# Optimization experiments

Measured on AMD Instinct MI355X. Metric: run time of the kernel, lower is better.

Reference implementation:

```python
import jax, jax.numpy as jnp
import numpy as np

EPS = 1e-7        # keras backend.epsilon()
TEMPERATURE = 0.1
MOMENTUM = 0.9
CENTROID_LR = 0.1
REPULSION_STRENGTH = 0.1
MIN_DISTANCE = 1.0

B, S, D = 8, 4096, 512
K = 512


def setup_inputs() -> dict:
    key = jax.random.key(0)
    kx, kc = jax.random.split(key)
    x = jax.random.normal(kx, (B, S, D), dtype=jnp.float32)
    # GlorotNormal for (K, D) centroid table
    glorot_std = float(np.sqrt(2.0 / (K + D)))
    centroids = jax.random.normal(kc, (K, D), dtype=jnp.float32) * glorot_std
    centroid_momentum = jnp.zeros((K, D), dtype=jnp.float32)
    return {"x": x, "centroids": centroids, "centroid_momentum": centroid_momentum}


def reference(x, centroids, centroid_momentum):
    # ---- flatten non-feature dims: (B, S, D) -> (N, D) ----
    flat = x.reshape(-1, x.shape[-1])                      # (N, D)

    # ---- squared Euclidean distances to centroids (GEMM form) ----
    x_sq = jnp.sum(flat * flat, axis=-1, keepdims=True)    # (N, 1)
    c_sq = jnp.sum(centroids * centroids, axis=-1)         # (K,)
    cross = flat @ centroids.T                             # (N, K)
    distances = x_sq + c_sq[None, :] - 2.0 * cross         # (N, K)

    # ---- temperature-scaled soft assignments (stable softmax w/ eps) ----
    scaled = -distances / TEMPERATURE
    scaled = scaled - jnp.max(scaled, axis=-1, keepdims=True)
    exp_d = jnp.exp(scaled)
    assignments = exp_d / (jnp.sum(exp_d, axis=-1, keepdims=True) + EPS)  # (N, K)

    # ---- soft K-means centroid targets ----
    sum_w = jnp.sum(assignments, axis=0)                   # (K,)
    weighted_sum = assignments.T @ flat                    # (K, D)
    new_centroids = weighted_sum / (sum_w[:, None] + EPS)  # (K, D)

    # ---- pairwise centroid repulsion ----
    diffs = centroids[:, None, :] - centroids[None, :, :]  # (K, K, D)
    sq_dist = jnp.sum(diffs * diffs, axis=-1)              # (K, K)
    dist = jnp.sqrt(sq_dist + EPS)
    rep_w = jnp.maximum(0.0, 1.0 - dist / MIN_DISTANCE)
    rep_scale = (REPULSION_STRENGTH * rep_w / (dist + EPS))[..., None]
    repulsion = jnp.sum(rep_scale * diffs, axis=1)         # (K, D)

    # ---- momentum update of centroids ----
    updates = new_centroids - centroids + repulsion
    mom_new = MOMENTUM * centroid_momentum + (1.0 - MOMENTUM) * updates
    centroids_new = centroids + CENTROID_LR * mom_new

    # ---- output: assignments reshaped to (B, S, K) ----
    out = assignments.reshape(x.shape[:-1] + (assignments.shape[-1],))
    return out, centroids_new, mom_new
```

## Files before the change

kernel.cpp:

```cpp
#include <hip/hip_runtime.h>
#include <hip/hip_bf16.h>

#define EPSF 1e-7f

typedef __attribute__((ext_vector_type(8))) short bf16x8;
typedef __attribute__((ext_vector_type(4))) float f32x4v;

__device__ inline ushort f2bf_bits(float x) {
    union { __hip_bfloat16 b; ushort u; } cv;
    cv.b = __float2bfloat16(x);
    return cv.u;
}
__device__ inline float bfbits2f(ushort u) {
    union { ushort u; __hip_bfloat16 b; } cv;
    cv.u = u;
    return __bfloat162float(cv.b);
}
__device__ inline void split2(float x, ushort& h, ushort& l) {
    h = f2bf_bits(x);
    l = f2bf_bits(x - bfbits2f(h));
}
__device__ inline uint4 pack8(const ushort* h) {
    uint4 p;
    p.x = (uint)h[0] | ((uint)h[1] << 16);
    p.y = (uint)h[2] | ((uint)h[3] << 16);
    p.z = (uint)h[4] | ((uint)h[5] << 16);
    p.w = (uint)h[6] | ((uint)h[7] << 16);
    return p;
}

__device__ inline void gload_lds16(const ushort* g, ushort* l) {
    __builtin_amdgcn_global_load_lds(
        (const __attribute__((address_space(1))) unsigned int*)g,
        (__attribute__((address_space(3))) unsigned int*)l, 16, 0, 0);
}

__global__ __launch_bounds__(256) void csqc_v3(const float* __restrict__ C,
                                               float* __restrict__ csq,
                                               ushort* __restrict__ Chl) {
    const int wave = threadIdx.x >> 6, lane = threadIdx.x & 63;
    const int row = blockIdx.x * 4 + wave;
    const int kc = lane >> 2, s = lane & 3;
    const float* p = C + row * 512 + lane * 8;
    float4 a = *(const float4*)p;
    float4 b = *(const float4*)(p + 4);
    float v[8] = {a.x, a.y, a.z, a.w, b.x, b.y, b.z, b.w};
    ushort h[8], l[8];
    float sqs = 0.f;
#pragma unroll
    for (int i = 0; i < 8; ++i) {
        sqs += v[i] * v[i];
        split2(v[i], h[i], l[i]);
    }
    ushort* base = Chl + (long)row * 1024 + kc * 64 + s * 8;
    *(uint4*)base = pack8(h);
    *(uint4*)(base + 32) = pack8(l);
#pragma unroll
    for (int off = 1; off < 64; off <<= 1) sqs += __shfl_xor(sqs, off, 64);
    if (lane == 0) csq[row] = sqs;
}

__global__ __launch_bounds__(512) void logsm(const float* __restrict__ X,
                                             const ushort* __restrict__ Chl,
                                             const float* __restrict__ csq,
                                             float* __restrict__ assign,
                                             ushort* __restrict__ Abf,
                                             ushort* __restrict__ Xh,
                                             float* __restrict__ sum_w) {
    __shared__ __align__(16) ushort sA[64 * 64];
    __shared__ __align__(16) ushort sB[512 * 64];
    __shared__ float rmaxs[64][4];
    __shared__ float rsums[64][4];
    __shared__ float swacc[512];
    const int tid = threadIdx.x;
    const int m0 = ((blockIdx.x & 7) * 64 + (blockIdx.x >> 3)) * 64;
    const int wid = tid >> 6, lane = tid & 63;
    const int wm = wid >> 2, wn = wid & 3;
    const int lrow = lane & 15, lkb = lane >> 4;
    swacc[tid] = 0.f;
    f32x4v acc[2][8] = {};

    const int ar = tid >> 3, aq = tid & 7;
    const float* xrow = X + (long)(m0 + ar) * 512 + aq * 4;
    float4 v = *(const float4*)xrow;

#pragma unroll 1
    for (int kc = 0; kc < 16; ++kc) {
        __syncthreads();
        {
            ushort h[4], l[4];
            split2(v.x, h[0], l[0]);
            split2(v.y, h[1], l[1]);
            split2(v.z, h[2], l[2]);
            split2(v.w, h[3], l[3]);
            ushort4 hv = {h[0], h[1], h[2], h[3]};
            ushort4 lv = {l[0], l[1], l[2], l[3]};
            const int sh = (aq >> 1) ^ (ar & 7);
            const int slo = ((aq >> 1) + 4) ^ (ar & 7);
            *(ushort4*)&sA[ar * 64 + (sh << 3) + (aq & 1) * 4] = hv;
            *(ushort4*)&sA[ar * 64 + (slo << 3) + (aq & 1) * 4] = lv;
            *(ushort4*)(Xh + (long)(m0 + ar) * 512 + kc * 32 + aq * 4) = hv;
        }
#pragma unroll
        for (int i = 0; i < 8; ++i) {
            const int sl = i * 512 + tid;
            const int r = sl >> 3, j = sl & 7;
            const int s = j ^ (r & 7);
            gload_lds16(Chl + (long)r * 1024 + kc * 64 + s * 8,
                        &sB[(i * 512 + wid * 64) * 8]);
        }
        if (kc < 15) v = *(const float4*)(xrow + (kc + 1) * 32);
        __syncthreads();
        bf16x8 ah[2], al[2];
#pragma unroll
        for (int mi = 0; mi < 2; ++mi) {
            const int R = wm * 32 + mi * 16 + lrow;
            ah[mi] = *(const bf16x8*)&sA[R * 64 + ((lkb ^ (R & 7)) << 3)];
            al[mi] = *(const bf16x8*)&sA[R * 64 + (((lkb + 4) ^ (R & 7)) << 3)];
        }
#pragma unroll
        for (int ni = 0; ni < 8; ++ni) {
            const int Rn = wn * 128 + ni * 16 + lrow;
            bf16x8 bh = *(const bf16x8*)&sB[Rn * 64 + ((lkb ^ (Rn & 7)) << 3)];
            bf16x8 bl = *(const bf16x8*)&sB[Rn * 64 + (((lkb + 4) ^ (Rn & 7)) << 3)];
#pragma unroll
            for (int mi = 0; mi < 2; ++mi) {
                acc[mi][ni] = __builtin_amdgcn_mfma_f32_16x16x32_bf16(ah[mi], bh, acc[mi][ni], 0, 0, 0);
                acc[mi][ni] = __builtin_amdgcn_mfma_f32_16x16x32_bf16(ah[mi], bl, acc[mi][ni], 0, 0, 0);
                acc[mi][ni] = __builtin_amdgcn_mfma_f32_16x16x32_bf16(al[mi], bh, acc[mi][ni], 0, 0, 0);
            }
        }
    }
    const int colb = wn * 128 + lrow;
    float cs[8];
#pragma unroll
    for (int ni = 0; ni < 8; ++ni) cs[ni] = csq[colb + ni * 16];
    float mx[2][4];
#pragma unroll
    for (int mi = 0; mi < 2; ++mi)
#pragma unroll
        for (int r = 0; r < 4; ++r) {
            float m = -3.0e38f;
#pragma unroll
            for (int ni = 0; ni < 8; ++ni) {
                float l = 2.0f * acc[mi][ni][r] - cs[ni];
                acc[mi][ni][r] = l;
                m = fmaxf(m, l);
            }
            mx[mi][r] = m;
        }
#pragma unroll
    for (int off = 1; off < 16; off <<= 1)
#pragma unroll
        for (int mi = 0; mi < 2; ++mi)
#pragma unroll
            for (int r = 0; r < 4; ++r) mx[mi][r] = fmaxf(mx[mi][r], __shfl_xor(mx[mi][r], off, 64));
    if (lrow == 0) {
#pragma unroll
        for (int mi = 0; mi < 2; ++mi)
#pragma unroll
            for (int r = 0; r < 4; ++r) rmaxs[wm * 32 + mi * 16 + lkb * 4 + r][wn] = mx[mi][r];
    }
    __syncthreads();
    float gmax[2][4];
#pragma unroll
    for (int mi = 0; mi < 2; ++mi)
#pragma unroll
        for (int r = 0; r < 4; ++r) {
            const int row = wm * 32 + mi * 16 + lkb * 4 + r;
            gmax[mi][r] = fmaxf(fmaxf(rmaxs[row][0], rmaxs[row][1]),
                                fmaxf(rmaxs[row][2], rmaxs[row][3]));
        }
    float sm[2][4] = {};
#pragma unroll
    for (int mi = 0; mi < 2; ++mi)
#pragma unroll
        for (int ni = 0; ni < 8; ++ni)
#pragma unroll
            for (int r = 0; r < 4; ++r) {
                float e = expf((acc[mi][ni][r] - gmax[mi][r]) * 10.0f);
                acc[mi][ni][r] = e;
                sm[mi][r] += e;
            }
#pragma unroll
    for (int off = 1; off < 16; off <<= 1)
#pragma unroll
        for (int mi = 0; mi < 2; ++mi)
#pragma unroll
            for (int r = 0; r < 4; ++r) sm[mi][r] += __shfl_xor(sm[mi][r], off, 64);
    if (lrow == 0) {
#pragma unroll
        for (int mi = 0; mi < 2; ++mi)
#pragma unroll
            for (int r = 0; r < 4; ++r) rsums[wm * 32 + mi * 16 + lkb * 4 + r][wn] = sm[mi][r];
    }
    __syncthreads();
    float inv[2][4];
#pragma unroll
    for (int mi = 0; mi < 2; ++mi)
#pragma unroll
        for (int r = 0; r < 4; ++r) {
            const int row = wm * 32 + mi * 16 + lkb * 4 + r;
            float t = rsums[row][0] + rsums[row][1] + rsums[row][2] + rsums[row][3];
            inv[mi][r] = 1.0f / (t + EPSF);
        }
    float csum[8] = {};
#pragma unroll
    for (int mi = 0; mi < 2; ++mi)
#pragma unroll
        for (int ni = 0; ni < 8; ++ni) {
            const int col = colb + ni * 16;
#pragma unroll
            for (int r = 0; r < 4; ++r) {
                const int row = wm * 32 + mi * 16 + lkb * 4 + r;
                float a = acc[mi][ni][r] * inv[mi][r];
                assign[(long)(m0 + row) * 512 + col] = a;
                Abf[(long)(m0 + row) * 512 + col] = f2bf_bits(a);
                csum[ni] += a;
            }
        }
#pragma unroll
    for (int off = 16; off < 64; off <<= 1)
#pragma unroll
        for (int ni = 0; ni < 8; ++ni) csum[ni] += __shfl_xor(csum[ni], off, 64);
    if (lkb == 0) {
#pragma unroll
        for (int ni = 0; ni < 8; ++ni) atomicAdd(&swacc[colb + ni * 16], csum[ni]);
    }
    __syncthreads();
    atomicAdd(&sum_w[tid], swacc[tid]);
}

__global__ __launch_bounds__(256) void gram_s_v3(const ushort* __restrict__ Chl,
                                                 const float* __restrict__ csq,
                                                 float* __restrict__ S,
                                                 float* __restrict__ rsum) {
    __shared__ __align__(16) ushort sA[128 * 64];
    __shared__ __align__(16) ushort sB[128 * 64];
    __shared__ float rs_s[128];
    const int tid = threadIdx.x;
    const int n0 = blockIdx.x * 128;
    const int m0 = blockIdx.y * 128;
    const int wid = tid >> 6, lane = tid & 63;
    const int wm = wid >> 1, wn = wid & 1;
    const int lrow = lane & 15, lkb = lane >> 4;
    f32x4v acc[4][4] = {};

#pragma unroll 1
    for (int kc = 0; kc < 16; ++kc) {
        __syncthreads();
#pragma unroll
        for (int i = 0; i < 4; ++i) {
            const int sl = wid * 256 + i * 64 + lane;
            const int r = sl >> 3, j = sl & 7;
            const int s = j ^ (r & 7);
            gload_lds16(Chl + (long)(m0 + r) * 1024 + kc * 64 + s * 8,
                        &sA[(wid * 256 + i * 64) * 8]);
            gload_lds16(Chl + (long)(n0 + r) * 1024 + kc * 64 + s * 8,
                        &sB[(wid * 256 + i * 64) * 8]);
        }
        __syncthreads();
        bf16x8 ah[4], al[4], bh[4], bl[4];
#pragma unroll
        for (int mi = 0; mi < 4; ++mi) {
            const int R = wm * 64 + mi * 16 + lrow;
            ah[mi] = *(const bf16x8*)&sA[R * 64 + ((lkb ^ (R & 7)) << 3)];
            al[mi] = *(const bf16x8*)&sA[R * 64 + (((lkb + 4) ^ (R & 7)) << 3)];
        }
#pragma unroll
        for (int ni = 0; ni < 4; ++ni) {
            const int R = wn * 64 + ni * 16 + lrow;
            bh[ni] = *(const bf16x8*)&sB[R * 64 + ((lkb ^ (R & 7)) << 3)];
            bl[ni] = *(const bf16x8*)&sB[R * 64 + (((lkb + 4) ^ (R & 7)) << 3)];
        }
#pragma unroll
        for (int mi = 0; mi < 4; ++mi)
#pragma unroll
            for (int ni = 0; ni < 4; ++ni) {
                acc[mi][ni] = __builtin_amdgcn_mfma_f32_16x16x32_bf16(ah[mi], bh[ni], acc[mi][ni], 0, 0, 0);
                acc[mi][ni] = __builtin_amdgcn_mfma_f32_16x16x32_bf16(ah[mi], bl[ni], acc[mi][ni], 0, 0, 0);
                acc[mi][ni] = __builtin_amdgcn_mfma_f32_16x16x32_bf16(al[mi], bh[ni], acc[mi][ni], 0, 0, 0);
            }
    }
    if (tid < 128) rs_s[tid] = 0.f;
    __syncthreads();
    const int colb = n0 + wn * 64 + lrow;
    float csj[4];
#pragma unroll
    for (int ni = 0; ni < 4; ++ni) csj[ni] = csq[colb + ni * 16];
#pragma unroll
    for (int mi = 0; mi < 4; ++mi) {
        const int rowb = m0 + wm * 64 + mi * 16 + lkb * 4;
#pragma unroll
        for (int r = 0; r < 4; ++r) {
            const int row = rowb + r;
            const float csi = csq[row];
            float rowpart = 0.f;
#pragma unroll
            for (int ni = 0; ni < 4; ++ni) {
                const int col = colb + ni * 16;
                float sq = csi + csj[ni] - 2.0f * acc[mi][ni][r];
                float dist = sqrtf(fmaxf(sq, 0.f) + EPSF);
                float w = fmaxf(0.f, 1.f - dist);
                float sval = (row == col) ? 0.f : (0.1f * w / (dist + EPSF));
                S[(long)row * 512 + col] = sval;
                rowpart += sval;
            }
            atomicAdd(&rs_s[row - m0], rowpart);
        }
    }
    __syncthreads();
    if (tid < 128) atomicAdd(&rsum[m0 + tid], rs_s[tid]);
}

__global__ __launch_bounds__(256) void wsum_v3(const ushort* __restrict__ Abf,
                                               const ushort* __restrict__ Xh,
                                               float* __restrict__ WSp) {
    __shared__ __align__(16) ushort sA[2][128 * 64];
    __shared__ __align__(16) ushort sB[2][128 * 64];
    const int tid = threadIdx.x;
    const int lin = blockIdx.x + blockIdx.y * 4 + blockIdx.z * 16;
    const int T = (lin & 7) * 64 + (lin >> 3);
    const int k0 = (T & 3) * 128;
    const int d0 = ((T >> 2) & 3) * 128;
    const int zc = T >> 4;
    const long n0 = (long)zc * 1024;
    const int wid = tid >> 6, lane = tid & 63;
    const int wm = wid >> 1, wn = wid & 1;
    const int lrow = lane & 15, lkb = lane >> 4;
    f32x4v acc[4][4] = {};

    const int c0_ = tid & 127, no0 = tid >> 7;
    ushort ha[4][8], hx[4][8];

#define WSUM_LOAD(NCOFF)                                                      \
    {                                                                          \
        _Pragma("unroll")                                                      \
        for (int it = 0; it < 4; ++it) {                                       \
            const int idx = it * 256 + tid;                                    \
            const int c = idx & 127;                                           \
            const int no = idx >> 7;                                           \
            const long nb = n0 + (NCOFF) + (long)no * 8;                       \
            _Pragma("unroll")                                                  \
            for (int jj = 0; jj < 8; ++jj) {                                   \
                ha[it][jj] = Abf[(nb + jj) * 512 + k0 + c];                    \
                hx[it][jj] = Xh[(nb + jj) * 512 + d0 + c];                     \
            }                                                                  \
        }                                                                      \
    }
#define WSUM_WRITE(B)                                                         \
    {                                                                          \
        _Pragma("unroll")                                                      \
        for (int it = 0; it < 4; ++it) {                                       \
            const int idx = it * 256 + tid;                                    \
            const int c = idx & 127;                                           \
            const int no = idx >> 7;                                           \
            const int sl = no ^ (c & 7);                                       \
            *(uint4*)&sA[(B)][c * 64 + sl * 8] = pack8(ha[it]);                \
            *(uint4*)&sB[(B)][c * 64 + sl * 8] = pack8(hx[it]);                \
        }                                                                      \
    }

    WSUM_LOAD(0);
    WSUM_WRITE(0);
    int cur = 0;
#pragma unroll 1
    for (int nc = 0; nc < 16; ++nc) {
        if (nc < 15) WSUM_LOAD((nc + 1) * 64);
        __syncthreads();
#pragma unroll
        for (int kk = 0; kk < 2; ++kk) {
            const int j = kk * 4 + lkb;
            bf16x8 af[4], bfv[4];
#pragma unroll
            for (int mi = 0; mi < 4; ++mi) {
                const int R = wm * 64 + mi * 16 + lrow;
                af[mi] = *(const bf16x8*)&sA[cur][R * 64 + ((j ^ (R & 7)) << 3)];
            }
#pragma unroll
            for (int ni = 0; ni < 4; ++ni) {
                const int R = wn * 64 + ni * 16 + lrow;
                bfv[ni] = *(const bf16x8*)&sB[cur][R * 64 + ((j ^ (R & 7)) << 3)];
            }
#pragma unroll
            for (int mi = 0; mi < 4; ++mi)
#pragma unroll
                for (int ni = 0; ni < 4; ++ni)
                    acc[mi][ni] = __builtin_amdgcn_mfma_f32_16x16x32_bf16(af[mi], bfv[ni], acc[mi][ni], 0, 0, 0);
        }
        if (nc < 15) WSUM_WRITE(cur ^ 1);
        cur ^= 1;
    }
    float* dst = WSp + (size_t)zc * 262144;
#pragma unroll
    for (int mi = 0; mi < 4; ++mi) {
        const int k = k0 + wm * 64 + mi * 16 + lkb * 4;
#pragma unroll
        for (int ni = 0; ni < 4; ++ni) {
            const int d = d0 + wn * 64 + ni * 16 + lrow;
#pragma unroll
            for (int r = 0; r < 4; ++r)
                dst[(k + r) * 512 + d] = acc[mi][ni][r];
        }
    }
#undef WSUM_LOAD
#undef WSUM_WRITE
}

__global__ __launch_bounds__(256) void apply_update(const float* __restrict__ Cent,
                                                    const float* __restrict__ Mom,
                                                    const float* __restrict__ S,
                                                    const float* __restrict__ rsum,
                                                    const float* __restrict__ WSp,
                                                    const float* __restrict__ sum_w,
                                                    float* __restrict__ outC,
                                                    float* __restrict__ outM) {
    const int i = blockIdx.x;
    __shared__ float srow[512];
    __shared__ int nz;
    const int tid = threadIdx.x;
    if (tid == 0) nz = 0;
    __syncthreads();
    float2 sv = *(const float2*)(S + (long)i * 512 + tid * 2);
    srow[tid * 2] = sv.x;
    srow[tid * 2 + 1] = sv.y;
    if (sv.x != 0.f || sv.y != 0.f) nz = 1;
    __syncthreads();
    const float rs = rsum[i];
    const float invw = 1.0f / (sum_w[i] + EPSF);
    const int d0 = tid * 2;
    float ws0 = 0.f, ws1 = 0.f;
#pragma unroll 4
    for (int z = 0; z < 32; ++z) {
        float2 w = *(const float2*)(WSp + (size_t)z * 262144 + (long)i * 512 + d0);
        ws0 += w.x;
        ws1 += w.y;
    }
    float sc0 = 0.f, sc1 = 0.f;
    if (nz) {
        for (int j = 0; j < 512; ++j) {
            const float s = srow[j];
            if (s != 0.f) {
                sc0 += s * Cent[(long)j * 512 + d0];
                sc1 += s * Cent[(long)j * 512 + d0 + 1];
            }
        }
    }
    float2 ci = *(const float2*)(Cent + (long)i * 512 + d0);
    float2 mo = *(const float2*)(Mom + (long)i * 512 + d0);
    float rep0 = rs * ci.x - sc0;
    float rep1 = rs * ci.y - sc1;
    float mn0 = 0.9f * mo.x + 0.1f * (ws0 * invw - ci.x + rep0);
    float mn1 = 0.9f * mo.y + 0.1f * (ws1 * invw - ci.y + rep1);
    float2 om = {mn0, mn1};
    float2 oc = {ci.x + 0.1f * mn0, ci.y + 0.1f * mn1};
    *(float2*)(outM + (long)i * 512 + d0) = om;
    *(float2*)(outC + (long)i * 512 + d0) = oc;
}

__global__ __launch_bounds__(256) void csq_only(const float* __restrict__ C,
                                                float* __restrict__ csq) {
    const int wave = threadIdx.x >> 6, lane = threadIdx.x & 63;
    const int row = blockIdx.x * 4 + wave;
    const float* p = C + row * 512 + lane * 8;
    float4 a = *(const float4*)p;
    float4 b = *(const float4*)(p + 4);
    float s = a.x * a.x + a.y * a.y + a.z * a.z + a.w * a.w +
              b.x * b.x + b.y * b.y + b.z * b.z + b.w * b.w;
#pragma unroll
    for (int off = 1; off < 64; off <<= 1) s += __shfl_xor(s, off, 64);
    if (lane == 0) csq[row] = s;
}

__global__ __launch_bounds__(256) void logits_mfma(const float* __restrict__ X,
                                                   const float* __restrict__ Cm,
                                                   const float* __restrict__ csq,
                                                   float* __restrict__ L) {
    __shared__ ushort sAh[128][64];
    __shared__ ushort sAl[128][64];
    __shared__ ushort sBh[128][64];
    __shared__ ushort sBl[128][64];
    const int tid = threadIdx.x;
    const int m0 = blockIdx.x * 128;
    const int n0 = blockIdx.y * 128;
    const int wid = tid >> 6, lane = tid & 63;
    const int wm = wid >> 1, wn = wid & 1;
    const int lrow = lane & 15;
    const int lkb = lane >> 4;
    f32x4v acc[4][4] = {};
    for (int k0 = 0; k0 < 512; k0 += 64) {
        __syncthreads();
#pragma unroll
        for (int s = 0; s < 8; ++s) {
            const int idx = s * 256 + tid;
            const int r = idx >> 4;
            const int c4 = (idx & 15) << 2;
            const int e = c4 ^ ((r & 7) << 3);
            float4 va = *(const float4*)(X + (long)(m0 + r) * 512 + k0 + c4);
            ushort4 hh, ll;
            split2(va.x, hh.x, ll.x);
            split2(va.y, hh.y, ll.y);
            split2(va.z, hh.z, ll.z);
            split2(va.w, hh.w, ll.w);
            *(ushort4*)&sAh[r][e] = hh;
            *(ushort4*)&sAl[r][e] = ll;
            float4 vb = *(const float4*)(Cm + (long)(n0 + r) * 512 + k0 + c4);
            split2(vb.x, hh.x, ll.x);
            split2(vb.y, hh.y, ll.y);
            split2(vb.z, hh.z, ll.z);
            split2(vb.w, hh.w, ll.w);
            *(ushort4*)&sBh[r][e] = hh;
            *(ushort4*)&sBl[r][e] = ll;
        }
        __syncthreads();
#pragma unroll
        for (int kk = 0; kk < 2; ++kk) {
            const int ebase = kk * 32 + lkb * 8;
            bf16x8 ah[4], al[4], bh[4], bl[4];
#pragma unroll
            for (int mi = 0; mi < 4; ++mi) {
                const int R = wm * 64 + mi * 16 + lrow;
                const int e = ebase ^ ((R & 7) << 3);
                ah[mi] = *(const bf16x8*)&sAh[R][e];
                al[mi] = *(const bf16x8*)&sAl[R][e];
            }
#pragma unroll
            for (int ni = 0; ni < 4; ++ni) {
                const int Rn = wn * 64 + ni * 16 + lrow;
                const int e = ebase ^ ((Rn & 7) << 3);
                bh[ni] = *(const bf16x8*)&sBh[Rn][e];
                bl[ni] = *(const bf16x8*)&sBl[Rn][e];
            }
#pragma unroll
            for (int mi = 0; mi < 4; ++mi)
#pragma unroll
                for (int ni = 0; ni < 4; ++ni) {
                    acc[mi][ni] = __builtin_amdgcn_mfma_f32_16x16x32_bf16(ah[mi], bh[ni], acc[mi][ni], 0, 0, 0);
                    acc[mi][ni] = __builtin_amdgcn_mfma_f32_16x16x32_bf16(ah[mi], bl[ni], acc[mi][ni], 0, 0, 0);
                    acc[mi][ni] = __builtin_amdgcn_mfma_f32_16x16x32_bf16(al[mi], bh[ni], acc[mi][ni], 0, 0, 0);
                }
        }
    }
    const int colb = n0 + wn * 64 + lrow;
    float cs[4];
#pragma unroll
    for (int ni = 0; ni < 4; ++ni) cs[ni] = csq[colb + ni * 16];
#pragma unroll
    for (int mi = 0; mi < 4; ++mi) {
        const int rowb = m0 + wm * 64 + mi * 16 + lkb * 4;
#pragma unroll
        for (int r = 0; r < 4; ++r) {
            float* Lp = L + (long)(rowb + r) * 512 + colb;
#pragma unroll
            for (int ni = 0; ni < 4; ++ni)
                Lp[ni * 16] = 2.0f * acc[mi][ni][r] - cs[ni];
        }
    }
}

__global__ __launch_bounds__(256) void softmax_rows(float* __restrict__ L,
                                                    float* __restrict__ sum_w,
                                                    ushort* __restrict__ Abf) {
    __shared__ float swacc[512];
    const int tid = threadIdx.x;
    for (int i = tid; i < 512; i += 256) swacc[i] = 0.f;
    __syncthreads();
    const int wave = tid >> 6, lane = tid & 63;
    float racc[8] = {};
    for (int r = blockIdx.x * 4 + wave; r < 32768; r += 2048) {
        float* p = L + (long)r * 512 + lane * 8;
        float4 v0 = *(float4*)p;
        float4 v1 = *(float4*)(p + 4);
        float v[8] = {v0.x, v0.y, v0.z, v0.w, v1.x, v1.y, v1.z, v1.w};
        float m = v[0];
#pragma unroll
        for (int i = 1; i < 8; ++i) m = fmaxf(m, v[i]);
#pragma unroll
        for (int off = 1; off < 64; off <<= 1) m = fmaxf(m, __shfl_xor(m, off, 64));
        float e[8], s = 0.f;
#pragma unroll
        for (int i = 0; i < 8; ++i) {
            e[i] = expf((v[i] - m) * 10.0f);
            s += e[i];
        }
#pragma unroll
        for (int off = 1; off < 64; off <<= 1) s += __shfl_xor(s, off, 64);
        const float inv = 1.0f / (s + EPSF);
        ushort eb[8];
#pragma unroll
        for (int i = 0; i < 8; ++i) {
            e[i] *= inv;
            racc[i] += e[i];
            eb[i] = f2bf_bits(e[i]);
        }
        float4 o0 = {e[0], e[1], e[2], e[3]};
        float4 o1 = {e[4], e[5], e[6], e[7]};
        *(float4*)p = o0;
        *(float4*)(p + 4) = o1;
        if (Abf) *(uint4*)(Abf + (long)r * 512 + lane * 8) = pack8(eb);
    }
#pragma unroll
    for (int i = 0; i < 8; ++i) atomicAdd(&swacc[lane * 8 + i], racc[i]);
    __syncthreads();
    for (int i = tid; i < 512; i += 256) atomicAdd(&sum_w[i], swacc[i]);
}

__global__ __launch_bounds__(256) void gemm_wsum(const float* __restrict__ A,
                                                 const float* __restrict__ X,
                                                 float* __restrict__ WS) {
    __shared__ float As[16][64];
    __shared__ float Xs[16][64];
    const int tid = threadIdx.x;
    const int tx = tid & 15, ty = tid >> 4;
    const int lrow = tid >> 4;
    const int lcol = (tid & 15) << 2;
    const int k0 = blockIdx.x * 64;
    const int d0 = blockIdx.y * 64;
    const int n0 = blockIdx.z * 1024;
    float acc[4][4] = {};
    for (int nc = 0; nc < 1024; nc += 16) {
        const long nrow = n0 + nc + lrow;
        float4 av = *(const float4*)(A + nrow * 512 + k0 + lcol);
        float4 xv = *(const float4*)(X + nrow * 512 + d0 + lcol);
        __syncthreads();
        *(float4*)&As[lrow][lcol] = av;
        *(float4*)&Xs[lrow][lcol] = xv;
        __syncthreads();
#pragma unroll
        for (int nn = 0; nn < 16; ++nn) {
            float4 a = *(const float4*)&As[nn][ty << 2];
            float4 x = *(const float4*)&Xs[nn][tx << 2];
            float aa[4] = {a.x, a.y, a.z, a.w};
            float xx[4] = {x.x, x.y, x.z, x.w};
#pragma unroll
            for (int i = 0; i < 4; ++i)
#pragma unroll
                for (int j = 0; j < 4; ++j) acc[i][j] += aa[i] * xx[j];
        }
    }
#pragma unroll
    for (int i = 0; i < 4; ++i)
#pragma unroll
        for (int j = 0; j < 4; ++j)
            atomicAdd(&WS[(k0 + (ty << 2) + i) * 512 + d0 + (tx << 2) + j], acc[i][j]);
}

__global__ __launch_bounds__(256) void repulse_update(const float* __restrict__ Cent,
                                                      const float* __restrict__ Mom,
                                                      const float* __restrict__ csq,
                                                      const float* __restrict__ WS,
                                                      const float* __restrict__ sum_w,
                                                      float* __restrict__ outC,
                                                      float* __restrict__ outM) {
    const int i = blockIdx.x;
    __shared__ float ci[512];
    __shared__ float rep[512];
    const int tid = threadIdx.x, wave = tid >> 6, lane = tid & 63;
    for (int d = tid; d < 512; d += 256) {
        ci[d] = Cent[i * 512 + d];
        rep[d] = 0.f;
    }
    __syncthreads();
    float cil[8];
#pragma unroll
    for (int m = 0; m < 8; ++m) cil[m] = ci[lane * 8 + m];
    const float csqi = csq[i];
    float racc[8] = {};
    for (int j = wave; j < 512; j += 4) {
        if (j == i) continue;
        const float* cj = Cent + j * 512 + lane * 8;
        float4 c0 = *(const float4*)cj;
        float4 c1 = *(const float4*)(cj + 4);
        float cjl[8] = {c0.x, c0.y, c0.z, c0.w, c1.x, c1.y, c1.z, c1.w};
        float dot = 0.f;
#pragma unroll
        for (int m = 0; m < 8; ++m) dot += cil[m] * cjl[m];
#pragma unroll
        for (int off = 1; off < 64; off <<= 1) dot += __shfl_xor(dot, off, 64);
        float sq = csqi + csq[j] - 2.f * dot;
        float dist = sqrtf(fmaxf(sq, 0.f) + EPSF);
        float w = fmaxf(0.f, 1.f - dist);
        float scale = 0.1f * w / (dist + EPSF);
#pragma unroll
        for (int m = 0; m < 8; ++m) racc[m] += scale * (cil[m] - cjl[m]);
    }
#pragma unroll
    for (int m = 0; m < 8; ++m) atomicAdd(&rep[lane * 8 + m], racc[m]);
    __syncthreads();
    const float invw = 1.0f / (sum_w[i] + EPSF);
    for (int d = tid; d < 512; d += 256) {
        float nc = WS[i * 512 + d] * invw;
        float upd = nc - ci[d] + rep[d];
        float mn = 0.9f * Mom[i * 512 + d] + 0.1f * upd;
        outM[i * 512 + d] = mn;
        outC[i * 512 + d] = ci[d] + 0.1f * mn;
    }
}

extern "C" void kernel_launch(void* const* d_in, const int* in_sizes, int n_in,
                              void* d_out, int out_size, void* d_ws, size_t ws_size,
                              hipStream_t stream) {
    const float* X = (const float*)d_in[0];
    const float* C = (const float*)d_in[1];
    const float* M = (const float*)d_in[2];
    float* out = (float*)d_out;
    float* assign = out;
    float* outC = out + 16777216;
    float* outM = outC + 262144;

    char* wsb = (char*)d_ws;
    const size_t MB = 1024ull * 1024ull;
    float* WS = (float*)wsb;
    float* sum_w = (float*)(wsb + 1 * MB);
    float* rsum = (float*)(wsb + 1 * MB + 2048);
    float* csq = (float*)(wsb + 1 * MB + 4096);
    ushort* Chl = (ushort*)(wsb + 2 * MB);
    float* S = (float*)(wsb + 3 * MB);
    float* WSp = (float*)(wsb + 4 * MB);
    ushort* Xh = (ushort*)(wsb + 36 * MB);
    ushort* Abf = (ushort*)(wsb + 100 * MB);
    const size_t NEED = 132 * MB;

    if (ws_size >= NEED) {
        hipMemsetAsync(wsb + 1 * MB, 0, 4096, stream);
        csqc_v3<<<128, 256, 0, stream>>>(C, csq, Chl);
        gram_s_v3<<<dim3(4, 4), 256, 0, stream>>>(Chl, csq, S, rsum);
        logsm<<<512, 512, 0, stream>>>(X, Chl, csq, assign, Abf, Xh, sum_w);
        wsum_v3<<<dim3(4, 4, 32), 256, 0, stream>>>(Abf, Xh, WSp);
        apply_update<<<512, 256, 0, stream>>>(C, M, S, rsum, WSp, sum_w, outC, outM);
    } else {
        hipMemsetAsync(d_ws, 0, 1 * MB + 8192, stream);
        csq_only<<<128, 256, 0, stream>>>(C, csq);
        logits_mfma<<<dim3(256, 4), 256, 0, stream>>>(X, C, csq, assign);
        softmax_rows<<<512, 256, 0, stream>>>(assign, sum_w, nullptr);
        gemm_wsum<<<dim3(8, 8, 32), 256, 0, stream>>>(assign, X, WS);
        repulse_update<<<512, 256, 0, stream>>>(C, M, csq, WS, sum_w, outC, outM);
    }
}
```

Before: 176.3 us.

## Merge centroid Gram kernel into weighted-sum kernel launch and drop X prefetch

Folds the 16-block centroid Gram/repulsion kernel into the weighted-sum GEMM launch as 16 extra blocks, so it runs alongside that work instead of as its own small, poorly occupied launch. This removes one kernel launch and the serialized gap it caused. Inside logsm, the register prefetch of the next X chunk is removed and the load is done at the top of each iteration. That shortens live ranges but exposes global load latency. The Gram blocks now run in the tail of a 528-block grid and reuse the double-buffer LDS sizing, which raises that path's shared memory footprint.

```diff
diff --git a/kernel.cpp b/kernel.cpp
--- a/kernel.cpp
+++ b/kernel.cpp
@@ -81,13 +81,12 @@
     f32x4v acc[2][8] = {};
 
     const int ar = tid >> 3, aq = tid & 7;
-    const float* xrow = X + (long)(m0 + ar) * 512 + aq * 4;
-    float4 v = *(const float4*)xrow;
 
 #pragma unroll 1
     for (int kc = 0; kc < 16; ++kc) {
         __syncthreads();
         {
+            float4 v = *(const float4*)(X + (long)(m0 + ar) * 512 + kc * 32 + aq * 4);
             ushort h[4], l[4];
             split2(v.x, h[0], l[0]);
             split2(v.y, h[1], l[1]);
@@ -109,7 +108,6 @@
             gload_lds16(Chl + (long)r * 1024 + kc * 64 + s * 8,
                         &sB[(i * 512 + wid * 64) * 8]);
         }
-        if (kc < 15) v = *(const float4*)(xrow + (kc + 1) * 32);
         __syncthreads();
         bf16x8 ah[2], al[2];
 #pragma unroll
@@ -231,180 +229,173 @@
     atomicAdd(&sum_w[tid], swacc[tid]);
 }
 
-__global__ __launch_bounds__(256) void gram_s_v3(const ushort* __restrict__ Chl,
+__global__ __launch_bounds__(256) void wsum_gram(const ushort* __restrict__ Abf,
+                                                 const ushort* __restrict__ Xh,
+                                                 float* __restrict__ WSp,
+                                                 const ushort* __restrict__ Chl,
                                                  const float* __restrict__ csq,
                                                  float* __restrict__ S,
                                                  float* __restrict__ rsum) {
-    __shared__ __align__(16) ushort sA[128 * 64];
-    __shared__ __align__(16) ushort sB[128 * 64];
+    __shared__ __align__(16) ushort sA[2][128 * 64];
+    __shared__ __align__(16) ushort sB[2][128 * 64];
     __shared__ float rs_s[128];
     const int tid = threadIdx.x;
-    const int n0 = blockIdx.x * 128;
-    const int m0 = blockIdx.y * 128;
+    const int bid = blockIdx.x;
     const int wid = tid >> 6, lane = tid & 63;
     const int wm = wid >> 1, wn = wid & 1;
     const int lrow = lane & 15, lkb = lane >> 4;
     f32x4v acc[4][4] = {};
 
+    if (bid < 512) {
+        const int T = (bid & 7) * 64 + (bid >> 3);
+        const int k0 = (T & 3) * 128;
+        const int d0 = ((T >> 2) & 3) * 128;
+        const int zc = T >> 4;
+        const long n0 = (long)zc * 1024;
+        ushort ha[4][8], hx[4][8];
+
+#define WSUM_LOAD(NCOFF)                                                      \
+        {                                                                      \
+            _Pragma("unroll")                                                  \
+            for (int it = 0; it < 4; ++it) {                                   \
+                const int idx = it * 256 + tid;                                \
+                const int c = idx & 127;                                       \
+                const int no = idx >> 7;                                       \
+                const long nb = n0 + (NCOFF) + (long)no * 8;                   \
+                _Pragma("unroll")                                              \
+                for (int jj = 0; jj < 8; ++jj) {                               \
+                    ha[it][jj] = Abf[(nb + jj) * 512 + k0 + c];                \
+                    hx[it][jj] = Xh[(nb + jj) * 512 + d0 + c];                 \
+                }                                                              \
+            }                                                                  \
+        }
+#define WSUM_WRITE(B)                                                         \
+        {                                                                      \
+            _Pragma("unroll")                                                  \
+            for (int it = 0; it < 4; ++it) {                                   \
+                const int idx = it * 256 + tid;                                \
+                const int c = idx & 127;                                       \
+                const int no = idx >> 7;                                       \
+                const int sl = no ^ (c & 7);                                   \
+                *(uint4*)&sA[(B)][c * 64 + sl * 8] = pack8(ha[it]);            \
+                *(uint4*)&sB[(B)][c * 64 + sl * 8] = pack8(hx[it]);            \
+            }                                                                  \
+        }
+
+        WSUM_LOAD(0);
+        WSUM_WRITE(0);
+        int cur = 0;
 #pragma unroll 1
-    for (int kc = 0; kc < 16; ++kc) {
-        __syncthreads();
-#pragma unroll
-        for (int i = 0; i < 4; ++i) {
-            const int sl = wid * 256 + i * 64 + lane;
-            const int r = sl >> 3, j = sl & 7;
-            const int s = j ^ (r & 7);
-            gload_lds16(Chl + (long)(m0 + r) * 1024 + kc * 64 + s * 8,
-                        &sA[(wid * 256 + i * 64) * 8]);
-            gload_lds16(Chl + (long)(n0 + r) * 1024 + kc * 64 + s * 8,
-                        &sB[(wid * 256 + i * 64) * 8]);
-        }
-        __syncthreads();
-        bf16x8 ah[4], al[4], bh[4], bl[4];
+        for (int nc = 0; nc < 16; ++nc) {
+            if (nc < 15) WSUM_LOAD((nc + 1) * 64);
+            __syncthreads();
+#pragma unroll
+            for (int kk = 0; kk < 2; ++kk) {
+                const int j = kk * 4 + lkb;
+                bf16x8 af[4], bfv[4];
+#pragma unroll
+                for (int mi = 0; mi < 4; ++mi) {
+                    const int R = wm * 64 + mi * 16 + lrow;
+                    af[mi] = *(const bf16x8*)&sA[cur][R * 64 + ((j ^ (R & 7)) << 3)];
+                }
+#pragma unroll
+                for (int ni = 0; ni < 4; ++ni) {
+                    const int R = wn * 64 + ni * 16 + lrow;
+                    bfv[ni] = *(const bf16x8*)&sB[cur][R * 64 + ((j ^ (R & 7)) << 3)];
+                }
+#pragma unroll
+                for (int mi = 0; mi < 4; ++mi)
+#pragma unroll
+                    for (int ni = 0; ni < 4; ++ni)
+                        acc[mi][ni] = __builtin_amdgcn_mfma_f32_16x16x32_bf16(af[mi], bfv[ni], acc[mi][ni], 0, 0, 0);
+            }
+            if (nc < 15) WSUM_WRITE(cur ^ 1);
+            cur ^= 1;
+        }
+        float* dst = WSp + (size_t)zc * 262144;
 #pragma unroll
         for (int mi = 0; mi < 4; ++mi) {
-            const int R = wm * 64 + mi * 16 + lrow;
-            ah[mi] = *(const bf16x8*)&sA[R * 64 + ((lkb ^ (R & 7)) << 3)];
-            al[mi] = *(const bf16x8*)&sA[R * 64 + (((lkb + 4) ^ (R & 7)) << 3)];
-        }
-#pragma unroll
-        for (int ni = 0; ni < 4; ++ni) {
-            const int R = wn * 64 + ni * 16 + lrow;
-            bh[ni] = *(const bf16x8*)&sB[R * 64 + ((lkb ^ (R & 7)) << 3)];
-            bl[ni] = *(const bf16x8*)&sB[R * 64 + (((lkb + 4) ^ (R & 7)) << 3)];
-        }
-#pragma unroll
-        for (int mi = 0; mi < 4; ++mi)
+            const int k = k0 + wm * 64 + mi * 16 + lkb * 4;
 #pragma unroll
             for (int ni = 0; ni < 4; ++ni) {
-                acc[mi][ni] = __builtin_amdgcn_mfma_f32_16x16x32_bf16(ah[mi], bh[ni], acc[mi][ni], 0, 0, 0);
-                acc[mi][ni] = __builtin_amdgcn_mfma_f32_16x16x32_bf16(ah[mi], bl[ni], acc[mi][ni], 0, 0, 0);
-                acc[mi][ni] = __builtin_amdgcn_mfma_f32_16x16x32_bf16(al[mi], bh[ni], acc[mi][ni], 0, 0, 0);
-            }
-    }
-    if (tid < 128) rs_s[tid] = 0.f;
-    __syncthreads();
-    const int colb = n0 + wn * 64 + lrow;
-    float csj[4];
-#pragma unroll
-    for (int ni = 0; ni < 4; ++ni) csj[ni] = csq[colb + ni * 16];
-#pragma unroll
-    for (int mi = 0; mi < 4; ++mi) {
-        const int rowb = m0 + wm * 64 + mi * 16 + lkb * 4;
-#pragma unroll
-        for (int r = 0; r < 4; ++r) {
-            const int row = rowb + r;
-            const float csi = csq[row];
-            float rowpart = 0.f;
-#pragma unroll
-            for (int ni = 0; ni < 4; ++ni) {
-                const int col = colb + ni * 16;
-                float sq = csi + csj[ni] - 2.0f * acc[mi][ni][r];
-                float dist = sqrtf(fmaxf(sq, 0.f) + EPSF);
-                float w = fmaxf(0.f, 1.f - dist);
-                float sval = (row == col) ? 0.f : (0.1f * w / (dist + EPSF));
-                S[(long)row * 512 + col] = sval;
-                rowpart += sval;
-            }
-            atomicAdd(&rs_s[row - m0], rowpart);
-        }
-    }
-    __syncthreads();
-    if (tid < 128) atomicAdd(&rsum[m0 + tid], rs_s[tid]);
-}
-
-__global__ __launch_bounds__(256) void wsum_v3(const ushort* __restrict__ Abf,
-                                               const ushort* __restrict__ Xh,
-                                               float* __restrict__ WSp) {
-    __shared__ __align__(16) ushort sA[2][128 * 64];
-    __shared__ __align__(16) ushort sB[2][128 * 64];
-    const int tid = threadIdx.x;
-    const int lin = blockIdx.x + blockIdx.y * 4 + blockIdx.z * 16;
-    const int T = (lin & 7) * 64 + (lin >> 3);
-    const int k0 = (T & 3) * 128;
-    const int d0 = ((T >> 2) & 3) * 128;
-    const int zc = T >> 4;
-    const long n0 = (long)zc * 1024;
-    const int wid = tid >> 6, lane = tid & 63;
-    const int wm = wid >> 1, wn = wid & 1;
-    const int lrow = lane & 15, lkb = lane >> 4;
-    f32x4v acc[4][4] = {};
-
-    const int c0_ = tid & 127, no0 = tid >> 7;
-    ushort ha[4][8], hx[4][8];
-
-#define WSUM_LOAD(NCOFF)                                                      \
-    {                                                                          \
-        _Pragma("unroll")                                                      \
-        for (int it = 0; it < 4; ++it) {                                       \
-            const int idx = it * 256 + tid;                                    \
-            const int c = idx & 127;                                           \
-            const int no = idx >> 7;                                           \
-            const long nb = n0 + (NCOFF) + (long)no * 8;                       \
-            _Pragma("unroll")                                                  \
-            for (int jj = 0; jj < 8; ++jj) {                                   \
-                ha[it][jj] = Abf[(nb + jj) * 512 + k0 + c];                    \
-                hx[it][jj] = Xh[(nb + jj) * 512 + d0 + c];                     \
-            }                                                                  \
-        }                                                                      \
-    }
-#define WSUM_WRITE(B)                                                         \
-    {                                                                          \
-        _Pragma("unroll")                                                      \
-        for (int it = 0; it < 4; ++it) {                                       \
-            const int idx = it * 256 + tid;                                    \
-            const int c = idx & 127;                                           \
-            const int no = idx >> 7;                                           \
-            const int sl = no ^ (c & 7);                                       \
-            *(uint4*)&sA[(B)][c * 64 + sl * 8] = pack8(ha[it]);                \
-            *(uint4*)&sB[(B)][c * 64 + sl * 8] = pack8(hx[it]);                \
-        }                                                                      \
-    }
-
-    WSUM_LOAD(0);
-    WSUM_WRITE(0);
-    int cur = 0;
+                const int d = d0 + wn * 64 + ni * 16 + lrow;
+#pragma unroll
+                for (int r = 0; r < 4; ++r)
+                    dst[(k + r) * 512 + d] = acc[mi][ni][r];
+            }
+        }
+#undef WSUM_LOAD
+#undef WSUM_WRITE
+    } else {
+        const int g = bid - 512;
+        const int n0 = (g & 3) * 128;
+        const int m0 = (g >> 2) * 128;
 #pragma unroll 1
-    for (int nc = 0; nc < 16; ++nc) {
-        if (nc < 15) WSUM_LOAD((nc + 1) * 64);
-        __syncthreads();
-#pragma unroll
-        for (int kk = 0; kk < 2; ++kk) {
-            const int j = kk * 4 + lkb;
-            bf16x8 af[4], bfv[4];
+        for (int kc = 0; kc < 16; ++kc) {
+            __syncthreads();
+#pragma unroll
+            for (int i = 0; i < 4; ++i) {
+                const int sl = wid * 256 + i * 64 + lane;
+                const int r = sl >> 3, j = sl & 7;
+                const int s = j ^ (r & 7);
+                gload_lds16(Chl + (long)(m0 + r) * 1024 + kc * 64 + s * 8,
+                            &sA[0][(wid * 256 + i * 64) * 8]);
+                gload_lds16(Chl + (long)(n0 + r) * 1024 + kc * 64 + s * 8,
+                            &sB[0][(wid * 256 + i * 64) * 8]);
+            }
+            __syncthreads();
+            bf16x8 ah[4], al[4], bh[4], bl[4];
 #pragma unroll
             for (int mi = 0; mi < 4; ++mi) {
                 const int R = wm * 64 + mi * 16 + lrow;
-                af[mi] = *(const bf16x8*)&sA[cur][R * 64 + ((j ^ (R & 7)) << 3)];
+                ah[mi] = *(const bf16x8*)&sA[0][R * 64 + ((lkb ^ (R & 7)) << 3)];
+                al[mi] = *(const bf16x8*)&sA[0][R * 64 + (((lkb + 4) ^ (R & 7)) << 3)];
             }
 #pragma unroll
             for (int ni = 0; ni < 4; ++ni) {
                 const int R = wn * 64 + ni * 16 + lrow;
-                bfv[ni] = *(const bf16x8*)&sB[cur][R * 64 + ((j ^ (R & 7)) << 3)];
+                bh[ni] = *(const bf16x8*)&sB[0][R * 64 + ((lkb ^ (R & 7)) << 3)];
+                bl[ni] = *(const bf16x8*)&sB[0][R * 64 + (((lkb + 4) ^ (R & 7)) << 3)];
             }
 #pragma unroll
             for (int mi = 0; mi < 4; ++mi)
 #pragma unroll
-                for (int ni = 0; ni < 4; ++ni)
-                    acc[mi][ni] = __builtin_amdgcn_mfma_f32_16x16x32_bf16(af[mi], bfv[ni], acc[mi][ni], 0, 0, 0);
-        }
-        if (nc < 15) WSUM_WRITE(cur ^ 1);
-        cur ^= 1;
-    }
-    float* dst = WSp + (size_t)zc * 262144;
-#pragma unroll
-    for (int mi = 0; mi < 4; ++mi) {
-        const int k = k0 + wm * 64 + mi * 16 + lkb * 4;
-#pragma unroll
-        for (int ni = 0; ni < 4; ++ni) {
-            const int d = d0 + wn * 64 + ni * 16 + lrow;
-#pragma unroll
-            for (int r = 0; r < 4; ++r)
-                dst[(k + r) * 512 + d] = acc[mi][ni][r];
-        }
-    }
-#undef WSUM_LOAD
-#undef WSUM_WRITE
+                for (int ni = 0; ni < 4; ++ni) {
+                    acc[mi][ni] = __builtin_amdgcn_mfma_f32_16x16x32_bf16(ah[mi], bh[ni], acc[mi][ni], 0, 0, 0);
+                    acc[mi][ni] = __builtin_amdgcn_mfma_f32_16x16x32_bf16(ah[mi], bl[ni], acc[mi][ni], 0, 0, 0);
+                    acc[mi][ni] = __builtin_amdgcn_mfma_f32_16x16x32_bf16(al[mi], bh[ni], acc[mi][ni], 0, 0, 0);
+                }
+        }
+        if (tid < 128) rs_s[tid] = 0.f;
+        __syncthreads();
+        const int colb = n0 + wn * 64 + lrow;
+        float csj[4];
+#pragma unroll
+        for (int ni = 0; ni < 4; ++ni) csj[ni] = csq[colb + ni * 16];
+#pragma unroll
+        for (int mi = 0; mi < 4; ++mi) {
+            const int rowb = m0 + wm * 64 + mi * 16 + lkb * 4;
+#pragma unroll
+            for (int r = 0; r < 4; ++r) {
+                const int row = rowb + r;
+                const float csi = csq[row];
+                float rowpart = 0.f;
+#pragma unroll
+                for (int ni = 0; ni < 4; ++ni) {
+                    const int col = colb + ni * 16;
+                    float sq = csi + csj[ni] - 2.0f * acc[mi][ni][r];
+                    float dist = sqrtf(fmaxf(sq, 0.f) + EPSF);
+                    float w = fmaxf(0.f, 1.f - dist);
+                    float sval = (row == col) ? 0.f : (0.1f * w / (dist + EPSF));
+                    S[(long)row * 512 + col] = sval;
+                    rowpart += sval;
+                }
+                atomicAdd(&rs_s[row - m0], rowpart);
+            }
+        }
+        __syncthreads();
+        if (tid < 128) atomicAdd(&rsum[m0 + tid], rs_s[tid]);
+    }
 }
 
 __global__ __launch_bounds__(256) void apply_update(const float* __restrict__ Cent,
@@ -724,9 +715,8 @@
     if (ws_size >= NEED) {
         hipMemsetAsync(wsb + 1 * MB, 0, 4096, stream);
         csqc_v3<<<128, 256, 0, stream>>>(C, csq, Chl);
-        gram_s_v3<<<dim3(4, 4), 256, 0, stream>>>(Chl, csq, S, rsum);
         logsm<<<512, 512, 0, stream>>>(X, Chl, csq, assign, Abf, Xh, sum_w);
-        wsum_v3<<<dim3(4, 4, 32), 256, 0, stream>>>(Abf, Xh, WSp);
+        wsum_gram<<<528, 256, 0, stream>>>(Abf, Xh, WSp, Chl, csq, S, rsum);
         apply_update<<<512, 256, 0, stream>>>(C, M, S, rsum, WSp, sum_w, outC, outM);
     } else {
         hipMemsetAsync(d_ws, 0, 1 * MB + 8192, stream);
```

Measured after the change: 145.2 us. -17.6%, faster.
